# Kernel tuning notes

Hardware: AMD Instinct MI355X
Metric: run time of the kernel (lower is better)

The kernel has to match this reference:

```python
import jax, jax.numpy as jnp
import numpy as np

B, H, S, DK = 2, 8, 4096, 64


def setup_inputs() -> dict:
    key = jax.random.key(0)
    kq, kk, kv = jax.random.split(key, 3)
    Q = jax.random.normal(kq, (B, H, S, DK), dtype=jnp.float32)
    K = jax.random.normal(kk, (B, H, S, DK), dtype=jnp.float32)
    V = jax.random.normal(kv, (B, H, S, DK), dtype=jnp.float32)
    attn_mask = jnp.zeros((1,), dtype=bool)  # accepted but unused by the module
    return {"Q": Q, "K": K, "V": V, "attn_mask": attn_mask}


def reference(Q, K, V, attn_mask):
    d_k = Q.shape[-1]
    scale = 1.0 / np.sqrt(d_k).astype(np.float32)
    # scores: [b, h, q, k] -- full O(n^2) matrix, as in the original
    scores = jnp.einsum('bhqd,bhkd->bhqk', Q, K) * scale
    attn = jax.nn.softmax(scores, axis=-1)
    context = jnp.einsum('bhqk,bhkd->bhqd', attn, V)
    return (context, attn)
```

## Files before the change

kernel.cpp:

```cpp
#include <hip/hip_runtime.h>
#include <hip/hip_bf16.h>


typedef __bf16 bf16x8 __attribute__((ext_vector_type(8)));
typedef __bf16 bf16x4 __attribute__((ext_vector_type(4)));
typedef float f32x4 __attribute__((ext_vector_type(4)));

#define BH 16
#define SEQ 4096
#define DKD 64
#define PSTRIDE 72
#define LOG2E 1.44269504088896f

__global__ void cvt_bf16_kernel(const float* __restrict__ src,
                                __bf16* __restrict__ dst, int n4, float scale) {
    int i = blockIdx.x * blockDim.x + threadIdx.x;
    if (i < n4) {
        const float4 v = reinterpret_cast<const float4*>(src)[i];
        bf16x4 o;
        o[0] = (__bf16)(v.x * scale); o[1] = (__bf16)(v.y * scale);
        o[2] = (__bf16)(v.z * scale); o[3] = (__bf16)(v.w * scale);
        reinterpret_cast<bf16x4*>(dst)[i] = o;
    }
}

__global__ void transpose_v_kernel(const float* __restrict__ V,
                                   __bf16* __restrict__ Vt) {
    __shared__ __bf16 T[DKD][72];
    const int head = blockIdx.y;
    const int s0 = blockIdx.x * 64;
    const int t = threadIdx.x;
    const float* vp = V + ((size_t)head * SEQ + s0) * DKD;
#pragma unroll
    for (int i = 0; i < 16; ++i) {
        int j = i * 256 + t;
        T[j & 63][j >> 6] = (__bf16)vp[j];
    }
    __syncthreads();
    __bf16* op = Vt + (size_t)head * DKD * SEQ + s0;
#pragma unroll
    for (int i = 0; i < 16; ++i) {
        int j = i * 256 + t;
        op[(size_t)(j >> 6) * SEQ + (j & 63)] = T[j >> 6][j & 63];
    }
}

__global__ __launch_bounds__(128, 5) void attn_kernel(
    const __bf16* __restrict__ Qb, const __bf16* __restrict__ Kb,
    const __bf16* __restrict__ Vt, float* __restrict__ out_ctx,
    float* __restrict__ out_attn) {
    __shared__ __align__(16) __bf16 Pl[2][2][16][PSTRIDE];

    const int tid = threadIdx.x;
    const int w = tid >> 6;
    const int lane = tid & 63;
    const int c16 = lane & 15;
    const int g = lane >> 4;

    const int wg = blockIdx.x;
    const int head = ((wg & 7) << 1) | ((wg >> 3) & 1);
    const int qblk = wg >> 4;
    const int qbase = qblk * 32 + w * 16;

    const __bf16* qp = Qb + ((size_t)head * SEQ + qbase + c16) * DKD + g * 8;
    const bf16x8 qf0 = *reinterpret_cast<const bf16x8*>(qp);
    const bf16x8 qf1 = *reinterpret_cast<const bf16x8*>(qp + 32);

    const __bf16* kbase = Kb + (size_t)head * SEQ * DKD;
    const __bf16* vbase = Vt + (size_t)head * DKD * SEQ;
    float* attn_p = out_attn + ((size_t)head * SEQ + qbase) * SEQ;

    float lsum = 0.f;
    for (int t = 0; t < 64; ++t) {
        const int kt = t * 64;
#pragma unroll
        for (int ct = 0; ct < 4; ++ct) {
            const __bf16* kp = kbase + (size_t)(kt + ct * 16 + c16) * DKD + g * 8;
            bf16x8 kf0 = *reinterpret_cast<const bf16x8*>(kp);
            bf16x8 kf1 = *reinterpret_cast<const bf16x8*>(kp + 32);
            f32x4 a = (f32x4){0.f, 0.f, 0.f, 0.f};
            a = __builtin_amdgcn_mfma_f32_16x16x32_bf16(kf0, qf0, a, 0, 0, 0);
            a = __builtin_amdgcn_mfma_f32_16x16x32_bf16(kf1, qf1, a, 0, 0, 0);
            float e0 = __builtin_amdgcn_exp2f(a[0] * LOG2E);
            float e1 = __builtin_amdgcn_exp2f(a[1] * LOG2E);
            float e2 = __builtin_amdgcn_exp2f(a[2] * LOG2E);
            float e3 = __builtin_amdgcn_exp2f(a[3] * LOG2E);
            lsum += (e0 + e1) + (e2 + e3);
        }
    }
    lsum += __shfl_xor(lsum, 16);
    lsum += __shfl_xor(lsum, 32);
    const float inv_l = __builtin_amdgcn_rcpf(lsum);

    f32x4 o[4];
#pragma unroll
    for (int dt = 0; dt < 4; ++dt) o[dt] = (f32x4){0.f, 0.f, 0.f, 0.f};

    auto computeS = [&](int t, __bf16(*Pbuf)[PSTRIDE]) {
        const int kt = t * 64;
#pragma unroll
        for (int h = 0; h < 2; ++h) {
            f32x4 acc[2];
#pragma unroll
            for (int ct = 0; ct < 2; ++ct) {
                acc[ct] = (f32x4){0.f, 0.f, 0.f, 0.f};
                const __bf16* kp =
                    kbase + (size_t)(kt + h * 32 + ct * 16 + c16) * DKD + g * 8;
                bf16x8 kf0 = *reinterpret_cast<const bf16x8*>(kp);
                bf16x8 kf1 = *reinterpret_cast<const bf16x8*>(kp + 32);
                acc[ct] = __builtin_amdgcn_mfma_f32_16x16x32_bf16(kf0, qf0, acc[ct], 0, 0, 0);
                acc[ct] = __builtin_amdgcn_mfma_f32_16x16x32_bf16(kf1, qf1, acc[ct], 0, 0, 0);
            }
#pragma unroll
            for (int ct = 0; ct < 2; ++ct) {
                f32x4 p;
                bf16x4 pb;
#pragma unroll
                for (int r = 0; r < 4; ++r) {
                    p[r] = __builtin_amdgcn_exp2f(acc[ct][r] * LOG2E) * inv_l;
                    pb[r] = (__bf16)p[r];
                }
                *reinterpret_cast<f32x4*>(
                    attn_p + (size_t)c16 * SEQ + kt + h * 32 + ct * 16 + g * 4) = p;
                *reinterpret_cast<bf16x4*>(&Pbuf[c16][h * 32 + ct * 16 + g * 4]) = pb;
            }
        }
    };

    auto pvTile = [&](int t, const __bf16(*Pbuf)[PSTRIDE]) {
        const int kt = t * 64;
        bf16x8 pb0 = *reinterpret_cast<const bf16x8*>(&Pbuf[c16][g * 8]);
        bf16x8 pb1 = *reinterpret_cast<const bf16x8*>(&Pbuf[c16][g * 8 + 32]);
#pragma unroll
        for (int dt = 0; dt < 4; ++dt) {
            const __bf16* vp = vbase + (size_t)(dt * 16 + c16) * SEQ + kt + g * 8;
            bf16x8 vf0 = *reinterpret_cast<const bf16x8*>(vp);
            bf16x8 vf1 = *reinterpret_cast<const bf16x8*>(vp + 32);
            o[dt] = __builtin_amdgcn_mfma_f32_16x16x32_bf16(vf0, pb0, o[dt], 0, 0, 0);
            o[dt] = __builtin_amdgcn_mfma_f32_16x16x32_bf16(vf1, pb1, o[dt], 0, 0, 0);
        }
    };

    computeS(0, Pl[0][w]);
    for (int t = 1; t < 63; t += 2) {
        computeS(t, Pl[1][w]);
        pvTile(t - 1, Pl[0][w]);
        computeS(t + 1, Pl[0][w]);
        pvTile(t, Pl[1][w]);
    }
    computeS(63, Pl[1][w]);
    pvTile(62, Pl[0][w]);
    pvTile(63, Pl[1][w]);

    float* ctx_p = out_ctx + ((size_t)head * SEQ + qbase) * DKD;
#pragma unroll
    for (int dt = 0; dt < 4; ++dt)
        *reinterpret_cast<f32x4*>(ctx_p + (size_t)c16 * DKD + dt * 16 + g * 4) = o[dt];
}

extern "C" void kernel_launch(void* const* d_in, const int* in_sizes, int n_in,
                              void* d_out, int out_size, void* d_ws, size_t ws_size,
                              hipStream_t stream) {
    const float* Q = (const float*)d_in[0];
    const float* K = (const float*)d_in[1];
    const float* V = (const float*)d_in[2];
    float* out = (float*)d_out;

    const size_t nElem = (size_t)BH * SEQ * DKD;
    __bf16* Qb = (__bf16*)d_ws;
    __bf16* Kb = Qb + nElem;
    __bf16* Vt = Kb + nElem;

    float* out_ctx = out;
    float* out_attn = out + nElem;

    const int n4 = (int)(nElem / 4);
    cvt_bf16_kernel<<<dim3((n4 + 255) / 256), dim3(256), 0, stream>>>(Q, Qb, n4, 0.125f);
    cvt_bf16_kernel<<<dim3((n4 + 255) / 256), dim3(256), 0, stream>>>(K, Kb, n4, 1.0f);
    transpose_v_kernel<<<dim3(64, BH), dim3(256), 0, stream>>>(V, Vt);
    attn_kernel<<<dim3(BH * SEQ / 32), dim3(128), 0, stream>>>(Qb, Kb, Vt, out_ctx, out_attn);
}
```

Before: 803.7 us.

## Add producer/consumer warps: split row-sum pass and offload attn stores

Doubles the workgroup to four waves. All four split the first pass that computes softmax row sums across the key range, then combine the partial sums through shared memory. After that, two waves compute P and run the PV MFMAs, writing fp32 P into a double-buffered LDS tile. The other two waves copy that tile to the attention output in global memory, synchronised by per-tile barriers. The goal is to take the large attention-matrix global stores off the compute waves' critical path, at the cost of more LDS traffic, barriers every tile, and fewer resident blocks per CU.

```diff
diff --git a/kernel.cpp b/kernel.cpp
--- a/kernel.cpp
+++ b/kernel.cpp
@@ -9,7 +9,6 @@
 #define BH 16
 #define SEQ 4096
 #define DKD 64
-#define PSTRIDE 72
 #define LOG2E 1.44269504088896f
 
 __global__ void cvt_bf16_kernel(const float* __restrict__ src,
@@ -45,22 +44,25 @@
     }
 }
 
-__global__ __launch_bounds__(128, 5) void attn_kernel(
+__global__ __launch_bounds__(256, 4) void attn_kernel(
     const __bf16* __restrict__ Qb, const __bf16* __restrict__ Kb,
     const __bf16* __restrict__ Vt, float* __restrict__ out_ctx,
     float* __restrict__ out_attn) {
-    __shared__ __align__(16) __bf16 Pl[2][2][16][PSTRIDE];
+    __shared__ __align__(16) float Pf[2][2][16][68];
+    __shared__ float Lsum[4][16];
 
     const int tid = threadIdx.x;
     const int w = tid >> 6;
     const int lane = tid & 63;
     const int c16 = lane & 15;
     const int g = lane >> 4;
+    const int qsub = w & 1;
+    const int khalf = w >> 1;
 
     const int wg = blockIdx.x;
     const int head = ((wg & 7) << 1) | ((wg >> 3) & 1);
     const int qblk = wg >> 4;
-    const int qbase = qblk * 32 + w * 16;
+    const int qbase = qblk * 32 + qsub * 16;
 
     const __bf16* qp = Qb + ((size_t)head * SEQ + qbase + c16) * DKD + g * 8;
     const bf16x8 qf0 = *reinterpret_cast<const bf16x8*>(qp);
@@ -71,8 +73,8 @@
     float* attn_p = out_attn + ((size_t)head * SEQ + qbase) * SEQ;
 
     float lsum = 0.f;
-    for (int t = 0; t < 64; ++t) {
-        const int kt = t * 64;
+    for (int t = 0; t < 32; ++t) {
+        const int kt = (khalf * 32 + t) * 64;
 #pragma unroll
         for (int ct = 0; ct < 4; ++ct) {
             const __bf16* kp = kbase + (size_t)(kt + ct * 16 + c16) * DKD + g * 8;
@@ -90,72 +92,96 @@
     }
     lsum += __shfl_xor(lsum, 16);
     lsum += __shfl_xor(lsum, 32);
-    const float inv_l = __builtin_amdgcn_rcpf(lsum);
-
-    f32x4 o[4];
-#pragma unroll
-    for (int dt = 0; dt < 4; ++dt) o[dt] = (f32x4){0.f, 0.f, 0.f, 0.f};
-
-    auto computeS = [&](int t, __bf16(*Pbuf)[PSTRIDE]) {
-        const int kt = t * 64;
-#pragma unroll
-        for (int h = 0; h < 2; ++h) {
-            f32x4 acc[2];
-#pragma unroll
-            for (int ct = 0; ct < 2; ++ct) {
-                acc[ct] = (f32x4){0.f, 0.f, 0.f, 0.f};
-                const __bf16* kp =
-                    kbase + (size_t)(kt + h * 32 + ct * 16 + c16) * DKD + g * 8;
-                bf16x8 kf0 = *reinterpret_cast<const bf16x8*>(kp);
-                bf16x8 kf1 = *reinterpret_cast<const bf16x8*>(kp + 32);
-                acc[ct] = __builtin_amdgcn_mfma_f32_16x16x32_bf16(kf0, qf0, acc[ct], 0, 0, 0);
-                acc[ct] = __builtin_amdgcn_mfma_f32_16x16x32_bf16(kf1, qf1, acc[ct], 0, 0, 0);
-            }
-#pragma unroll
-            for (int ct = 0; ct < 2; ++ct) {
-                f32x4 p;
-                bf16x4 pb;
-#pragma unroll
-                for (int r = 0; r < 4; ++r) {
-                    p[r] = __builtin_amdgcn_exp2f(acc[ct][r] * LOG2E) * inv_l;
-                    pb[r] = (__bf16)p[r];
+    if (g == 0) Lsum[w][c16] = lsum;
+    __syncthreads();
+
+    if (w < 2) {
+        const float inv_l = __builtin_amdgcn_rcpf(Lsum[w][c16] + Lsum[w ^ 2][c16]);
+
+        f32x4 o[4];
+#pragma unroll
+        for (int dt = 0; dt < 4; ++dt) o[dt] = (f32x4){0.f, 0.f, 0.f, 0.f};
+
+        auto computeS = [&](int t, float(*Pbuf)[68]) {
+            const int kt = t * 64;
+#pragma unroll
+            for (int h = 0; h < 2; ++h) {
+                f32x4 acc[2];
+#pragma unroll
+                for (int ct = 0; ct < 2; ++ct) {
+                    acc[ct] = (f32x4){0.f, 0.f, 0.f, 0.f};
+                    const __bf16* kp =
+                        kbase + (size_t)(kt + h * 32 + ct * 16 + c16) * DKD + g * 8;
+                    bf16x8 kf0 = *reinterpret_cast<const bf16x8*>(kp);
+                    bf16x8 kf1 = *reinterpret_cast<const bf16x8*>(kp + 32);
+                    acc[ct] = __builtin_amdgcn_mfma_f32_16x16x32_bf16(kf0, qf0, acc[ct], 0, 0, 0);
+                    acc[ct] = __builtin_amdgcn_mfma_f32_16x16x32_bf16(kf1, qf1, acc[ct], 0, 0, 0);
                 }
-                *reinterpret_cast<f32x4*>(
-                    attn_p + (size_t)c16 * SEQ + kt + h * 32 + ct * 16 + g * 4) = p;
-                *reinterpret_cast<bf16x4*>(&Pbuf[c16][h * 32 + ct * 16 + g * 4]) = pb;
-            }
+#pragma unroll
+                for (int ct = 0; ct < 2; ++ct) {
+                    f32x4 p;
+#pragma unroll
+                    for (int r = 0; r < 4; ++r)
+                        p[r] = __builtin_amdgcn_exp2f(acc[ct][r] * LOG2E) * inv_l;
+                    *reinterpret_cast<f32x4*>(&Pbuf[c16][h * 32 + ct * 16 + g * 4]) = p;
+                }
+            }
+        };
+
+        auto pvTile = [&](int t, const float(*Pbuf)[68]) {
+            const int kt = t * 64;
+            f32x4 a0 = *reinterpret_cast<const f32x4*>(&Pbuf[c16][g * 8]);
+            f32x4 a1 = *reinterpret_cast<const f32x4*>(&Pbuf[c16][g * 8 + 4]);
+            f32x4 b0 = *reinterpret_cast<const f32x4*>(&Pbuf[c16][g * 8 + 32]);
+            f32x4 b1 = *reinterpret_cast<const f32x4*>(&Pbuf[c16][g * 8 + 36]);
+            bf16x8 pb0, pb1;
+#pragma unroll
+            for (int j = 0; j < 4; ++j) {
+                pb0[j] = (__bf16)a0[j]; pb0[j + 4] = (__bf16)a1[j];
+                pb1[j] = (__bf16)b0[j]; pb1[j + 4] = (__bf16)b1[j];
+            }
+#pragma unroll
+            for (int dt = 0; dt < 4; ++dt) {
+                const __bf16* vp = vbase + (size_t)(dt * 16 + c16) * SEQ + kt + g * 8;
+                bf16x8 vf0 = *reinterpret_cast<const bf16x8*>(vp);
+                bf16x8 vf1 = *reinterpret_cast<const bf16x8*>(vp + 32);
+                o[dt] = __builtin_amdgcn_mfma_f32_16x16x32_bf16(vf0, pb0, o[dt], 0, 0, 0);
+                o[dt] = __builtin_amdgcn_mfma_f32_16x16x32_bf16(vf1, pb1, o[dt], 0, 0, 0);
+            }
+        };
+
+        computeS(0, Pf[0][w]);
+        asm volatile("s_waitcnt lgkmcnt(0)" ::: "memory");
+        __builtin_amdgcn_s_barrier();
+        for (int t = 1; t < 64; ++t) {
+            computeS(t, Pf[t & 1][w]);
+            pvTile(t - 1, Pf[(t - 1) & 1][w]);
+            asm volatile("s_waitcnt lgkmcnt(0)" ::: "memory");
+            __builtin_amdgcn_s_barrier();
         }
-    };
-
-    auto pvTile = [&](int t, const __bf16(*Pbuf)[PSTRIDE]) {
-        const int kt = t * 64;
-        bf16x8 pb0 = *reinterpret_cast<const bf16x8*>(&Pbuf[c16][g * 8]);
-        bf16x8 pb1 = *reinterpret_cast<const bf16x8*>(&Pbuf[c16][g * 8 + 32]);
-#pragma unroll
-        for (int dt = 0; dt < 4; ++dt) {
-            const __bf16* vp = vbase + (size_t)(dt * 16 + c16) * SEQ + kt + g * 8;
-            bf16x8 vf0 = *reinterpret_cast<const bf16x8*>(vp);
-            bf16x8 vf1 = *reinterpret_cast<const bf16x8*>(vp + 32);
-            o[dt] = __builtin_amdgcn_mfma_f32_16x16x32_bf16(vf0, pb0, o[dt], 0, 0, 0);
-            o[dt] = __builtin_amdgcn_mfma_f32_16x16x32_bf16(vf1, pb1, o[dt], 0, 0, 0);
+        pvTile(63, Pf[1][w]);
+
+        float* ctx_p = out_ctx + ((size_t)head * SEQ + qbase) * DKD;
+#pragma unroll
+        for (int dt = 0; dt < 4; ++dt)
+            *reinterpret_cast<f32x4*>(ctx_p + (size_t)c16 * DKD + dt * 16 + g * 4) = o[dt];
+    } else {
+        const int srow = lane >> 2;
+        const int scN = (lane & 3) * 4;
+        const float* srcbase = &Pf[0][w & 1][0][0];
+        const float* srcalt = &Pf[1][w & 1][0][0];
+        for (int t = 0; t < 64; ++t) {
+            __builtin_amdgcn_s_barrier();
+            __builtin_amdgcn_sched_barrier(0);
+            const float* src = (t & 1) ? srcalt : srcbase;
+            const int kt = t * 64;
+#pragma unroll
+            for (int j = 0; j < 4; ++j) {
+                f32x4 v = *reinterpret_cast<const f32x4*>(src + srow * 68 + j * 16 + scN);
+                *reinterpret_cast<f32x4*>(attn_p + (size_t)srow * SEQ + kt + j * 16 + scN) = v;
+            }
         }
-    };
-
-    computeS(0, Pl[0][w]);
-    for (int t = 1; t < 63; t += 2) {
-        computeS(t, Pl[1][w]);
-        pvTile(t - 1, Pl[0][w]);
-        computeS(t + 1, Pl[0][w]);
-        pvTile(t, Pl[1][w]);
-    }
-    computeS(63, Pl[1][w]);
-    pvTile(62, Pl[0][w]);
-    pvTile(63, Pl[1][w]);
-
-    float* ctx_p = out_ctx + ((size_t)head * SEQ + qbase) * DKD;
-#pragma unroll
-    for (int dt = 0; dt < 4; ++dt)
-        *reinterpret_cast<f32x4*>(ctx_p + (size_t)c16 * DKD + dt * 16 + g * 4) = o[dt];
+    }
 }
 
 extern "C" void kernel_launch(void* const* d_in, const int* in_sizes, int n_in,
@@ -178,5 +204,5 @@
     cvt_bf16_kernel<<<dim3((n4 + 255) / 256), dim3(256), 0, stream>>>(Q, Qb, n4, 0.125f);
     cvt_bf16_kernel<<<dim3((n4 + 255) / 256), dim3(256), 0, stream>>>(K, Kb, n4, 1.0f);
     transpose_v_kernel<<<dim3(64, BH), dim3(256), 0, stream>>>(V, Vt);
-    attn_kernel<<<dim3(BH * SEQ / 32), dim3(128), 0, stream>>>(Qb, Kb, Vt, out_ctx, out_attn);
-}
+    attn_kernel<<<dim3(BH * SEQ / 32), dim3(256), 0, stream>>>(Qb, Kb, Vt, out_ctx, out_attn);
+}
```

Measured after the change: 775.9 us. -3.5%, faster.
